# Kernel tuning notes

Measured on AMD Instinct MI355X. Metric: run time of the kernel, lower is better.

Reference implementation:

```python
import jax, jax.numpy as jnp
import numpy as np

B, T, D = 4, 2048, 1024
H = 16
HD = D // H  # 64

def setup_inputs() -> dict:
    key = jax.random.key(0)
    k1, k2, k3, k4, k5 = jax.random.split(key, 5)
    s = 1.0 / np.sqrt(D)
    return {
        "x": jax.random.normal(k1, (B, T, D), dtype=jnp.float32),
        "Wqkv": jax.random.normal(k2, (D, 3 * D), dtype=jnp.float32) * s,
        "bqkv": jnp.zeros((3 * D,), dtype=jnp.float32),
        "Wproj": jax.random.normal(k3, (D, D), dtype=jnp.float32) * s,
        "bproj": jnp.zeros((D,), dtype=jnp.float32),
    }

def reference(x, Wqkv, bqkv, Wproj, bproj):
    Bq, Tq, C = x.shape
    qkv = x @ Wqkv + bqkv                       # [B,T,3D]
    qkv = qkv.reshape(Bq, Tq, 3, H, HD).transpose(2, 0, 3, 1, 4)  # [3,B,H,T,hd]
    q, k, v = qkv[0], qkv[1], qkv[2]
    scale = 1.0 / np.sqrt(HD)
    att = jnp.einsum("bhqd,bhkd->bhqk", q, k) * scale  # [B,H,T,T]
    causal = jnp.tril(jnp.ones((Tq, Tq), dtype=bool))
    att = jnp.where(causal[None, None], att, -jnp.inf)
    att = jax.nn.softmax(att, axis=-1)
    out = jnp.einsum("bhqk,bhkd->bhqd", att, v)        # [B,H,T,hd]
    out = out.transpose(0, 2, 1, 3).reshape(Bq, Tq, C)
    return out @ Wproj + bproj
```

## Files before the change

### kernel.cpp

```cpp
#include <hip/hip_runtime.h>

typedef float f32x4 __attribute__((ext_vector_type(4)));
typedef __bf16 bf16x8 __attribute__((ext_vector_type(8)));
typedef __bf16 bf16x4 __attribute__((ext_vector_type(4)));

#define B_ 4
#define T_ 2048
#define D_ 1024
#define H_ 16
#define HD_ 64

__device__ __forceinline__ void gload_lds16(const void* g, void* l) {
  __builtin_amdgcn_global_load_lds(
      (const __attribute__((address_space(1))) void*)g,
      (__attribute__((address_space(3))) void*)l, 16, 0, 0);
}

__global__ __launch_bounds__(256) void k_cvt_f32_bf16(
    const float* __restrict__ in, __bf16* __restrict__ out, int n4) {
  int i = blockIdx.x * blockDim.x + threadIdx.x;
  int stride = gridDim.x * blockDim.x;
  for (; i < n4; i += stride) {
    float4 v = reinterpret_cast<const float4*>(in)[i];
    bf16x4 o = { (__bf16)v.x, (__bf16)v.y, (__bf16)v.z, (__bf16)v.w };
    reinterpret_cast<bf16x4*>(out)[i] = o;
  }
}

template <typename Tin>
__global__ __launch_bounds__(256) void k_transpose_bf16(
    const Tin* __restrict__ in, __bf16* __restrict__ out,
    int R, int C, long inb, long outb) {
  __shared__ alignas(16) __bf16 lds[64 * 68];
  const int t = threadIdx.x;
  in  += (long)blockIdx.z * inb;
  out += (long)blockIdx.z * outb;
  const int r0 = blockIdx.y * 64, c0 = blockIdx.x * 64;
#pragma unroll
  for (int i = 0; i < 16; ++i) {
    int e = i * 256 + t, row = e >> 6, col = e & 63;
    lds[row * 68 + col] = (__bf16)(float)in[(long)(r0 + row) * C + c0 + col];
  }
  __syncthreads();
#pragma unroll
  for (int i = 0; i < 16; ++i) {
    int e = i * 256 + t, orow = e >> 6, ocol = e & 63;
    out[(long)(c0 + orow) * R + r0 + ocol] = lds[ocol * 68 + orow];
  }
}

template <int EPI>
__global__ __launch_bounds__(256) void k_gemm_bt(
    const __bf16* __restrict__ A, const __bf16* __restrict__ Bt,
    const float* __restrict__ bias, void* __restrict__ Cout,
    __bf16* __restrict__ vout, int M, int N, int K) {
  __shared__ alignas(16) __bf16 As[2][128 * 32];
  __shared__ alignas(16) __bf16 Bs[2][128 * 32];
  const int t = threadIdx.x;
  const int w = t >> 6, l = t & 63;
  const int g = l >> 4, r16 = l & 15;
  const int wr = w >> 1, wc = w & 1;
  const int m0 = blockIdx.y * 128, n0 = blockIdx.x * 128;

  f32x4 acc[4][4];
#pragma unroll
  for (int i = 0; i < 4; ++i)
#pragma unroll
    for (int j = 0; j < 4; ++j) acc[i][j] = (f32x4){0.f, 0.f, 0.f, 0.f};

  const int arow = t >> 2;
  const int acol = ((t & 3) ^ ((t >> 3) & 3)) * 8;
  const char* Ag = (const char*)(A + (long)(m0 + arow) * K + acol);
  const char* Bg = (const char*)(Bt + (long)(n0 + arow) * K + acol);
  const long rowskip = (long)64 * K * 2;
  const int rdsw = (g ^ ((r16 >> 1) & 3)) * 8;

  auto stage = [&](int buf, long koff) {
    char* AsW = (char*)As[buf] + w * 1024;
    char* BsW = (char*)Bs[buf] + w * 1024;
    gload_lds16(Ag + koff, AsW);
    gload_lds16(Ag + koff + rowskip, AsW + 4096);
    gload_lds16(Bg + koff, BsW);
    gload_lds16(Bg + koff + rowskip, BsW + 4096);
  };

  stage(0, 0);
  __syncthreads();

  for (int kt = 0; kt < K; kt += 32) {
    const int cur = (kt >> 5) & 1;
    if (kt + 32 < K) stage(cur ^ 1, (long)(kt + 32) * 2);
    bf16x8 af[4], bfr[4];
#pragma unroll
    for (int mi = 0; mi < 4; ++mi)
      af[mi] = *reinterpret_cast<const bf16x8*>(
          &As[cur][(wr * 64 + mi * 16 + r16) * 32 + rdsw]);
#pragma unroll
    for (int ni = 0; ni < 4; ++ni)
      bfr[ni] = *reinterpret_cast<const bf16x8*>(
          &Bs[cur][(wc * 64 + ni * 16 + r16) * 32 + rdsw]);
    __builtin_amdgcn_s_setprio(1);
#pragma unroll
    for (int mi = 0; mi < 4; ++mi)
#pragma unroll
      for (int ni = 0; ni < 4; ++ni)
        acc[mi][ni] = __builtin_amdgcn_mfma_f32_16x16x32_bf16(af[mi], bfr[ni], acc[mi][ni], 0, 0, 0);
    __builtin_amdgcn_s_setprio(0);
    __syncthreads();
  }

  if (EPI == 0) {
    const int which = n0 >> 10;
    __bf16* qkvb = (__bf16*)Cout;
#pragma unroll
    for (int mi = 0; mi < 4; ++mi) {
#pragma unroll
      for (int ni = 0; ni < 4; ++ni) {
        const int n = n0 + wc * 64 + ni * 16 + r16;
        const float bv = bias[n];
        f32x4 c = acc[mi][ni];
        const int rem = n & 1023, h = rem >> 6, hd = rem & 63;
        const int mbase = m0 + wr * 64 + mi * 16 + g * 4;
        const int b = mbase >> 11, tt0 = mbase & 2047;
        if (which < 2) {
#pragma unroll
          for (int r = 0; r < 4; ++r)
            qkvb[((long)((which * B_ + b) * H_ + h) * T_ + tt0 + r) * HD_ + hd] =
                (__bf16)(c[r] + bv);
        } else {
          bf16x4 pk = { (__bf16)(c[0] + bv), (__bf16)(c[1] + bv),
                        (__bf16)(c[2] + bv), (__bf16)(c[3] + bv) };
          *reinterpret_cast<bf16x4*>(
              &vout[(((long)b * H_ + h) * HD_ + hd) * T_ + tt0]) = pk;
        }
      }
    }
  } else {
    float* O = (float*)Cout;
#pragma unroll
    for (int mi = 0; mi < 4; ++mi) {
#pragma unroll
      for (int ni = 0; ni < 4; ++ni) {
        const int n = n0 + wc * 64 + ni * 16 + r16;
        const float bv = bias[n];
        f32x4 c = acc[mi][ni];
        const int mbase = m0 + wr * 64 + mi * 16 + g * 4;
#pragma unroll
        for (int r = 0; r < 4; ++r) O[(long)(mbase + r) * N + n] = c[r] + bv;
      }
    }
  }
}

__device__ __forceinline__ void soft_side(
    const f32x4 (&s)[4], float& lrun, bool diag, int qrel,
    int g, int r16, bf16x8& pa0, bf16x8& pa1) {
  float p[4][4];
#pragma unroll
  for (int nf = 0; nf < 4; ++nf) {
#pragma unroll
    for (int rr = 0; rr < 4; ++rr) {
      float x = s[nf][rr];
      if (diag) x = (nf * 16 + 4 * g + rr <= qrel + r16) ? x : -1e30f;
      p[nf][rr] = exp2f(x);
    }
  }
  const float ps0 = (p[0][0] + p[0][1]) + (p[0][2] + p[0][3]);
  const float ps1 = (p[1][0] + p[1][1]) + (p[1][2] + p[1][3]);
  const float ps2 = (p[2][0] + p[2][1]) + (p[2][2] + p[2][3]);
  const float ps3 = (p[3][0] + p[3][1]) + (p[3][2] + p[3][3]);
  lrun += (ps0 + ps1) + (ps2 + ps3);

  unsigned u[4][2];
#pragma unroll
  for (int nf = 0; nf < 4; ++nf) {
    asm("v_cvt_pk_bf16_f32 %0, %1, %2"
        : "=v"(u[nf][0]) : "v"(p[nf][0]), "v"(p[nf][1]));
    asm("v_cvt_pk_bf16_f32 %0, %1, %2"
        : "=v"(u[nf][1]) : "v"(p[nf][2]), "v"(p[nf][3]));
  }
#pragma unroll
  for (int j = 0; j < 2; ++j) {
    asm("v_permlane32_swap_b32 %0, %1" : "+v"(u[0][j]), "+v"(u[1][j]));
    asm("v_permlane32_swap_b32 %0, %1" : "+v"(u[2][j]), "+v"(u[3][j]));
  }
#pragma unroll
  for (int j = 0; j < 2; ++j) {
    asm("v_permlane16_swap_b32 %0, %1" : "+v"(u[0][j]), "+v"(u[1][j]));
    asm("v_permlane16_swap_b32 %0, %1" : "+v"(u[2][j]), "+v"(u[3][j]));
  }
  union PU { unsigned w[4]; bf16x8 v; };
  PU a0, a1;
  a0.w[0] = u[0][0]; a0.w[1] = u[0][1]; a0.w[2] = u[1][0]; a0.w[3] = u[1][1];
  a1.w[0] = u[2][0]; a1.w[1] = u[2][1]; a1.w[2] = u[3][0]; a1.w[3] = u[3][1];
  pa0 = a0.v;
  pa1 = a1.v;
}

__global__ __launch_bounds__(256) void k_attn(
    const __bf16* __restrict__ q, const __bf16* __restrict__ k,
    const __bf16* __restrict__ vt, __bf16* __restrict__ o) {
  __shared__ alignas(16) __bf16 Ks[2][64 * 64];
  __shared__ alignas(16) __bf16 Vs[2][64 * 64];
  const int t = threadIdx.x, w = t >> 6, l = t & 63;
  const int g = l >> 4, r16 = l & 15;
  const int bh = blockIdx.x;
  const int prmap[16] = {0, 2, 4, 6, 15, 13, 11, 9, 1, 3, 5, 7, 14, 12, 10, 8};
  const int pr = prmap[blockIdx.y];
  const int qtA = 31 - pr, qtB = pr;
  const int qbaseA = qtA * 64 + w * 16;
  const int qbaseB = qtB * 64 + w * 16;
  const float sc = 0.125f * 1.44269504088896341f;

  auto scale8 = [&](bf16x8 v) {
    bf16x8 r;
#pragma unroll
    for (int j = 0; j < 8; ++j) r[j] = (__bf16)((float)v[j] * sc);
    return r;
  };
  const __bf16* qpA = q + ((long)bh * T_ + qbaseA + r16) * HD_ + g * 8;
  const bf16x8 aqA0 = scale8(*reinterpret_cast<const bf16x8*>(qpA));
  const bf16x8 aqA1 = scale8(*reinterpret_cast<const bf16x8*>(qpA + 32));
  const __bf16* qpB = q + ((long)bh * T_ + qbaseB + r16) * HD_ + g * 8;
  const bf16x8 aqB0 = scale8(*reinterpret_cast<const bf16x8*>(qpB));
  const bf16x8 aqB1 = scale8(*reinterpret_cast<const bf16x8*>(qpB + 32));

  f32x4 oA[4], oB[4];
  float lA = 0.f, lB = 0.f;
#pragma unroll
  for (int i = 0; i < 4; ++i) {
    oA[i] = (f32x4){0.f, 0.f, 0.f, 0.f};
    oB[i] = (f32x4){0.f, 0.f, 0.f, 0.f};
  }

  const int srow = t >> 3, sslot = t & 7;
  const int sswz = sslot ^ (srow & 7);
  const char* kg = (const char*)(k + ((long)bh * T_ + srow) * HD_) + sswz * 16;
  const char* vg = (const char*)(vt + ((long)bh * HD_ + srow) * T_) + sswz * 16;

  auto stage = [&](int buf, int kv0) {
    char* Kd = (char*)Ks[buf] + w * 1024;
    char* Vd = (char*)Vs[buf] + w * 1024;
    gload_lds16(kg + (long)kv0 * 128, Kd);
    gload_lds16(kg + (long)kv0 * 128 + 32 * 128, Kd + 4096);
    gload_lds16(vg + (long)kv0 * 2, Vd);
    gload_lds16(vg + (long)kv0 * 2 + 32 * (long)T_ * 2, Vd + 4096);
  };

  stage(0, 0);
  __syncthreads();

  const int ntile = qtA + 1;
  for (int it = 0; it < ntile; ++it) {
    const int cur = it & 1;
    if (it + 1 < ntile) stage(cur ^ 1, (it + 1) * 64);
    const char* Kc = (const char*)Ks[cur];
    const char* Vc = (const char*)Vs[cur];
    const bool doB = (it <= qtB);

    f32x4 sA[4], sB[4];
    __builtin_amdgcn_s_setprio(1);
#pragma unroll
    for (int nf = 0; nf < 4; ++nf) {
      const char* kb = Kc + (nf * 16 + r16) * 128;
      const bf16x8 b0 = *reinterpret_cast<const bf16x8*>(kb + ((g ^ (r16 & 7)) << 4));
      const bf16x8 b1 = *reinterpret_cast<const bf16x8*>(kb + (((4 + g) ^ (r16 & 7)) << 4));
      f32x4 z = (f32x4){0.f, 0.f, 0.f, 0.f};
      z = __builtin_amdgcn_mfma_f32_16x16x32_bf16(b0, aqA0, z, 0, 0, 0);
      z = __builtin_amdgcn_mfma_f32_16x16x32_bf16(b1, aqA1, z, 0, 0, 0);
      sA[nf] = z;
      if (doB) {
        f32x4 zb = (f32x4){0.f, 0.f, 0.f, 0.f};
        zb = __builtin_amdgcn_mfma_f32_16x16x32_bf16(b0, aqB0, zb, 0, 0, 0);
        zb = __builtin_amdgcn_mfma_f32_16x16x32_bf16(b1, aqB1, zb, 0, 0, 0);
        sB[nf] = zb;
      }
    }
    __builtin_amdgcn_s_setprio(0);

    bf16x8 paA0, paA1, paB0, paB1;
    soft_side(sA, lA, it == qtA, qbaseA - it * 64, g, r16, paA0, paA1);
    if (doB)
      soft_side(sB, lB, it == qtB, qbaseB - it * 64, g, r16, paB0, paB1);

    __builtin_amdgcn_s_setprio(1);
#pragma unroll
    for (int nf = 0; nf < 4; ++nf) {
      const char* vb = Vc + (nf * 16 + r16) * 128;
      const bf16x8 v0 = *reinterpret_cast<const bf16x8*>(vb + ((g ^ (r16 & 7)) << 4));
      const bf16x8 v1 = *reinterpret_cast<const bf16x8*>(vb + (((4 + g) ^ (r16 & 7)) << 4));
      oA[nf] = __builtin_amdgcn_mfma_f32_16x16x32_bf16(paA0, v0, oA[nf], 0, 0, 0);
      oA[nf] = __builtin_amdgcn_mfma_f32_16x16x32_bf16(paA1, v1, oA[nf], 0, 0, 0);
      if (doB) {
        oB[nf] = __builtin_amdgcn_mfma_f32_16x16x32_bf16(paB0, v0, oB[nf], 0, 0, 0);
        oB[nf] = __builtin_amdgcn_mfma_f32_16x16x32_bf16(paB1, v1, oB[nf], 0, 0, 0);
      }
    }
    __builtin_amdgcn_s_setprio(0);
    __syncthreads();
  }

  lA += __shfl_xor(lA, 16, 64);
  lA += __shfl_xor(lA, 32, 64);
  lB += __shfl_xor(lB, 16, 64);
  lB += __shfl_xor(lB, 32, 64);
  const float invA = 1.f / lA, invB = 1.f / lB;
  float invAq[4], invBq[4];
#pragma unroll
  for (int rr = 0; rr < 4; ++rr) {
    invAq[rr] = __shfl(invA, 4 * g + rr, 64);
    invBq[rr] = __shfl(invB, 4 * g + rr, 64);
  }
  const int b = bh >> 4, h = bh & 15;
#pragma unroll
  for (int nf = 0; nf < 4; ++nf) {
    const int hd = nf * 16 + r16;
#pragma unroll
    for (int rr = 0; rr < 4; ++rr) {
      const int ttA = qbaseA + g * 4 + rr;
      o[((long)b * T_ + ttA) * D_ + h * HD_ + hd] = (__bf16)(oA[nf][rr] * invAq[rr]);
      const int ttB = qbaseB + g * 4 + rr;
      o[((long)b * T_ + ttB) * D_ + h * HD_ + hd] = (__bf16)(oB[nf][rr] * invBq[rr]);
    }
  }
}

extern "C" void kernel_launch(void* const* d_in, const int* in_sizes, int n_in,
                              void* d_out, int out_size, void* d_ws, size_t ws_size,
                              hipStream_t stream) {
  (void)in_sizes; (void)n_in; (void)out_size; (void)ws_size;
  const float* x     = (const float*)d_in[0];
  const float* Wqkv  = (const float*)d_in[1];
  const float* bqkv  = (const float*)d_in[2];
  const float* Wproj = (const float*)d_in[3];
  const float* bproj = (const float*)d_in[4];
  float* out = (float*)d_out;

  const long MT = (long)B_ * T_;
  __bf16* xb     = (__bf16*)d_ws;
  __bf16* wqkvt  = xb + MT * D_;
  __bf16* wprojt = wqkvt + (long)3 * D_ * D_;
  __bf16* qkvb   = wprojt + (long)D_ * D_;
  __bf16* vtb    = qkvb + (long)2 * B_ * H_ * T_ * HD_;
  __bf16* attno  = vtb + (long)B_ * H_ * HD_ * T_;

  k_cvt_f32_bf16<<<2048, 256, 0, stream>>>(x, xb, (int)(MT * D_ / 4));
  k_transpose_bf16<float><<<dim3(48, 16, 1), 256, 0, stream>>>(Wqkv, wqkvt, D_, 3 * D_, 0, 0);
  k_transpose_bf16<float><<<dim3(16, 16, 1), 256, 0, stream>>>(Wproj, wprojt, D_, D_, 0, 0);
  k_gemm_bt<0><<<dim3(24, 64), 256, 0, stream>>>(xb, wqkvt, bqkv, qkvb, vtb, 8192, 3072, 1024);
  k_attn<<<dim3(64, 16), 256, 0, stream>>>(
      qkvb, qkvb + (long)B_ * H_ * T_ * HD_, vtb, attno);
  k_gemm_bt<1><<<dim3(8, 64), 256, 0, stream>>>(attno, wprojt, bproj, out, nullptr, 8192, 1024, 1024);
}
```

Measured before the change: 196.3 us.

## Shrink attention blocks to two waves with 32-row query tiles

The attention kernel now runs 128-thread blocks, each covering two 32-row query tiles (paired from opposite ends for causal balance) instead of two 64-row tiles with four waves. The grid doubles to 2048 blocks, and the two waves now stage the full 64x64 K/V tile with four async loads each. The aim is finer-grained work and better load balance and occupancy across CUs. The cost is that each staged K/V tile is reused by half as many query rows, so global/LDS traffic per FLOP roughly doubles. The hand-tuned block ordering map is also dropped.

```diff
diff --git a/kernel.cpp b/kernel.cpp
--- a/kernel.cpp
+++ b/kernel.cpp
@@ -197,19 +197,19 @@
   pa1 = a1.v;
 }
 
-__global__ __launch_bounds__(256) void k_attn(
+__global__ __launch_bounds__(128) void k_attn(
     const __bf16* __restrict__ q, const __bf16* __restrict__ k,
     const __bf16* __restrict__ vt, __bf16* __restrict__ o) {
   __shared__ alignas(16) __bf16 Ks[2][64 * 64];
   __shared__ alignas(16) __bf16 Vs[2][64 * 64];
   const int t = threadIdx.x, w = t >> 6, l = t & 63;
   const int g = l >> 4, r16 = l & 15;
-  const int bh = blockIdx.x;
-  const int prmap[16] = {0, 2, 4, 6, 15, 13, 11, 9, 1, 3, 5, 7, 14, 12, 10, 8};
-  const int pr = prmap[blockIdx.y];
-  const int qtA = 31 - pr, qtB = pr;
-  const int qbaseA = qtA * 64 + w * 16;
-  const int qbaseB = qtB * 64 + w * 16;
+  const int bh = blockIdx.x, pr = blockIdx.y;
+  const int tA = 63 - pr, tB = pr;
+  const int qbaseA = tA * 32 + w * 16;
+  const int qbaseB = tB * 32 + w * 16;
+  const int itLastA = (tA * 32 + 31) >> 6;
+  const int itLastB = (tB * 32 + 31) >> 6;
   const float sc = 0.125f * 1.44269504088896341f;
 
   auto scale8 = [&](bf16x8 v) {
@@ -233,30 +233,34 @@
     oB[i] = (f32x4){0.f, 0.f, 0.f, 0.f};
   }
 
-  const int srow = t >> 3, sslot = t & 7;
-  const int sswz = sslot ^ (srow & 7);
+  const int srow = l >> 3, sslot = l & 7;
+  const int sswz = sslot ^ srow;
   const char* kg = (const char*)(k + ((long)bh * T_ + srow) * HD_) + sswz * 16;
   const char* vg = (const char*)(vt + ((long)bh * HD_ + srow) * T_) + sswz * 16;
 
   auto stage = [&](int buf, int kv0) {
-    char* Kd = (char*)Ks[buf] + w * 1024;
-    char* Vd = (char*)Vs[buf] + w * 1024;
-    gload_lds16(kg + (long)kv0 * 128, Kd);
-    gload_lds16(kg + (long)kv0 * 128 + 32 * 128, Kd + 4096);
-    gload_lds16(vg + (long)kv0 * 2, Vd);
-    gload_lds16(vg + (long)kv0 * 2 + 32 * (long)T_ * 2, Vd + 4096);
+    char* Kd = (char*)Ks[buf];
+    char* Vd = (char*)Vs[buf];
+    const char* kgt = kg + (long)kv0 * 128;
+    const char* vgt = vg + (long)kv0 * 2;
+#pragma unroll
+    for (int c = 0; c < 4; ++c) {
+      const int slab = c * 2 + w;
+      gload_lds16(kgt + (long)slab * 8 * 128, Kd + slab * 1024);
+      gload_lds16(vgt + (long)slab * 8 * T_ * 2, Vd + slab * 1024);
+    }
   };
 
   stage(0, 0);
   __syncthreads();
 
-  const int ntile = qtA + 1;
+  const int ntile = itLastA + 1;
   for (int it = 0; it < ntile; ++it) {
     const int cur = it & 1;
     if (it + 1 < ntile) stage(cur ^ 1, (it + 1) * 64);
     const char* Kc = (const char*)Ks[cur];
     const char* Vc = (const char*)Vs[cur];
-    const bool doB = (it <= qtB);
+    const bool doB = (it <= itLastB);
 
     f32x4 sA[4], sB[4];
     __builtin_amdgcn_s_setprio(1);
@@ -279,9 +283,9 @@
     __builtin_amdgcn_s_setprio(0);
 
     bf16x8 paA0, paA1, paB0, paB1;
-    soft_side(sA, lA, it == qtA, qbaseA - it * 64, g, r16, paA0, paA1);
+    soft_side(sA, lA, it == itLastA, qbaseA - it * 64, g, r16, paA0, paA1);
     if (doB)
-      soft_side(sB, lB, it == qtB, qbaseB - it * 64, g, r16, paB0, paB1);
+      soft_side(sB, lB, it == itLastB, qbaseB - it * 64, g, r16, paB0, paB1);
 
     __builtin_amdgcn_s_setprio(1);
 #pragma unroll
@@ -348,7 +352,7 @@
   k_transpose_bf16<float><<<dim3(48, 16, 1), 256, 0, stream>>>(Wqkv, wqkvt, D_, 3 * D_, 0, 0);
   k_transpose_bf16<float><<<dim3(16, 16, 1), 256, 0, stream>>>(Wproj, wprojt, D_, D_, 0, 0);
   k_gemm_bt<0><<<dim3(24, 64), 256, 0, stream>>>(xb, wqkvt, bqkv, qkvb, vtb, 8192, 3072, 1024);
-  k_attn<<<dim3(64, 16), 256, 0, stream>>>(
+  k_attn<<<dim3(64, 32), 128, 0, stream>>>(
       qkvb, qkvb + (long)B_ * H_ * T_ * HD_, vtb, attno);
   k_gemm_bt<1><<<dim3(8, 64), 256, 0, stream>>>(attno, wprojt, bproj, out, nullptr, 8192, 1024, 1024);
 }
```

Result: slower. 221.1 us (+12.7%).
